# Kernel tuning notes

Measured on AMD Instinct MI355X. Metric: run time of the kernel, lower is better.

Reference implementation:

```python
import jax, jax.numpy as jnp
import numpy as np

K = 3          # kernel size
SH, SW = 2, 1  # stride
PH, PW = 1, 1  # padding


def conv2d(x, w, b, stride, pad):
    y = jax.lax.conv_general_dilated(
        x, w, window_strides=stride,
        padding=[(pad[0], pad[0]), (pad[1], pad[1])],
        dimension_numbers=('NCHW', 'OIHW', 'NCHW'))
    return y + b[None, :, None, None]


def setup_inputs() -> dict:
    key = jax.random.key(0)
    ks = jax.random.split(key, 4)
    x = jax.random.normal(ks[0], (8, 64, 128, 128), jnp.float32)
    # scale offset weights small so sampled offsets are O(1) pixels (exercises
    # the bilinear path without sampling far out of bounds)
    w_offset = jax.random.normal(ks[1], (18, 64, 3, 3), jnp.float32) * 0.02
    b_offset = jnp.zeros((18,), jnp.float32)
    w_mask = jax.random.normal(ks[2], (9, 64, 3, 3), jnp.float32) * 0.05
    b_mask = jnp.zeros((9,), jnp.float32)
    w_conv = jax.random.normal(ks[3], (64, 64, 3, 3), jnp.float32) * (1.0 / 24.0)
    return dict(x=x, w_offset=w_offset, b_offset=b_offset,
                w_mask=w_mask, b_mask=b_mask, w_conv=w_conv)


def _bilinear_gather(x, py, px):
    # x: [B,C,H,W]; py, px: [B,K2,Ho,Wo] float sampling coordinates.
    # Zero-padding outside the image (torchvision deform_conv2d semantics).
    B, C, H, W = x.shape
    y0f = jnp.floor(py)
    x0f = jnp.floor(px)
    dy = py - y0f
    dx = px - x0f
    y0 = y0f.astype(jnp.int32)
    x0 = x0f.astype(jnp.int32)

    def corner(yi, xi, wgt):
        valid = (yi >= 0) & (yi < H) & (xi >= 0) & (xi < W)
        yc = jnp.clip(yi, 0, H - 1)
        xc = jnp.clip(xi, 0, W - 1)
        # per-batch fancy gather -> [B, C, K2, Ho, Wo]
        g = jax.vmap(lambda xb, yb, xbi: xb[:, yb, xbi])(x, yc, xc)
        return g * (wgt * valid)[:, None]

    return (corner(y0,     x0,     (1 - dy) * (1 - dx))
            + corner(y0,     x0 + 1, (1 - dy) * dx)
            + corner(y0 + 1, x0,     dy * (1 - dx))
            + corner(y0 + 1, x0 + 1, dy * dx))


def reference(x, w_offset, b_offset, w_mask, b_mask, w_conv):
    B, C, H, W = x.shape
    offset = conv2d(x, w_offset, b_offset, (SH, SW), (PH, PW))   # [B, 2*K2, Ho, Wo]
    mask = jax.nn.sigmoid(conv2d(x, w_mask, b_mask, (SH, SW), (PH, PW)))  # [B, K2, Ho, Wo]
    Ho, Wo = offset.shape[2], offset.shape[3]
    K2 = K * K
    off = offset.reshape(B, K2, 2, Ho, Wo)
    off_y = off[:, :, 0]   # [B,K2,Ho,Wo]
    off_x = off[:, :, 1]
    ky = (jnp.arange(K2) // K).astype(jnp.float32)
    kx = (jnp.arange(K2) % K).astype(jnp.float32)
    hs = (jnp.arange(Ho) * SH - PH).astype(jnp.float32)
    ws = (jnp.arange(Wo) * SW - PW).astype(jnp.float32)
    py = off_y + ky[None, :, None, None] + hs[None, None, :, None]
    px = off_x + kx[None, :, None, None] + ws[None, None, None, :]
    sampled = _bilinear_gather(x, py, px) * mask[:, None]  # [B,C,K2,Ho,Wo]
    # weighted accumulate over in-channels and kernel taps
    out = jnp.einsum('ock,bckhw->bohw', w_conv.reshape(-1, C, K2), sampled)
    return out
```

## Files before the change

### kernel.cpp

```cpp
#include <hip/hip_runtime.h>
#include <hip/hip_fp16.h>
#include <math.h>

#define BB 8
#define CC 64
#define HH 128
#define WW 128
#define HO 64
#define WO 128
#define OC 64
#define HW (HH * WW)

typedef __attribute__((ext_vector_type(4))) float floatx4;
typedef __attribute__((ext_vector_type(8))) _Float16 half8;

__device__ __forceinline__ unsigned short f2h(float f) {
    __half h = __float2half(f);
    return __builtin_bit_cast(unsigned short, h);
}
__device__ __forceinline__ unsigned int packpair(float a, float b) {
    __half2 h = __floats2half2_rn(a, b);
    return __builtin_bit_cast(unsigned int, h);
}
__device__ __forceinline__ void lgkm_barrier() {
    asm volatile("s_waitcnt lgkmcnt(0)" ::: "memory");
    __builtin_amdgcn_s_barrier();
}

__global__ __launch_bounds__(256) void prep(
    const float* __restrict__ x,
    const float* __restrict__ w_off, const float* __restrict__ w_msk,
    const float* __restrict__ w_conv,
    unsigned int* __restrict__ xP,
    unsigned short* __restrict__ Wom, unsigned short* __restrict__ W2)
{
    __shared__ float T[66][65];
    int tid = threadIdx.x, bx = blockIdx.x;
    if (bx < 2048) {
        int wh = bx & 1, b = (bx >> 1) & 7, y = bx >> 4;
        int w0 = wh << 6;
        const float* xb = x + (((size_t)b * CC) * HH + y) * WW + w0;
#pragma unroll
        for (int i = 0; i < 4; ++i) {
            int idx = i * 256 + tid;
            int cch = idx >> 4, f4 = (idx & 15) << 2;
            floatx4 v = *(const floatx4*)(xb + (size_t)cch * HW + f4);
            T[f4 + 0][cch] = v.x;
            T[f4 + 1][cch] = v.y;
            T[f4 + 2][cch] = v.z;
            T[f4 + 3][cch] = v.w;
        }
        if (tid < 64) {
            float e = 0.0f;
            if (w0 + 64 < WW) e = xb[(size_t)tid * HW + 64];
            T[64][tid] = e;
        }
        __syncthreads();
        int c4 = tid & 15;
        int wr = tid >> 4;
        size_t rowbase = (((size_t)b * HH + y) * WW) + w0;
#pragma unroll
        for (int j = 0; j < 4; ++j) {
            int w = 16 * j + wr;
            floatx4 a  = *(const floatx4*)&T[w][4 * c4];
            floatx4 bb = *(const floatx4*)&T[w + 1][4 * c4];
            uint4 d;
            d.x = packpair(a.x, bb.x);
            d.y = packpair(a.y, bb.y);
            d.z = packpair(a.z, bb.z);
            d.w = packpair(a.w, bb.w);
            *(uint4*)(xP + (rowbase + w) * 64 + 4 * c4) = d;
        }
    } else if (bx < 2120) {
        int i = (bx - 2048) * 256 + tid;
        int chn = i / 576, kk = i % 576;
        int xs = kk >> 6, cc = kk & 63;
        float v = 0.0f;
        if (chn < 18)      v = w_off[(chn * CC + cc) * 9 + xs];
        else if (chn < 27) v = w_msk[((chn - 18) * CC + cc) * 9 + xs];
        Wom[i] = f2h(v);
    } else {
        int i = (bx - 2120) * 256 + tid;
        int k = i % 9, cc = (i / 9) % CC, o = i / (CC * 9);
        W2[((size_t)k * OC + o) * CC + cc] = f2h(w_conv[i]);
    }
}

__global__ __launch_bounds__(256, 4) void fused(
    const unsigned int* __restrict__ xP,
    const unsigned short* __restrict__ Wom, const unsigned short* __restrict__ W2,
    const float* __restrict__ b_off, const float* __restrict__ b_msk,
    float* __restrict__ out)
{
    __shared__ __align__(16) char lds[18304];
    typedef _Float16 XsRow[34][72];
    XsRow* Xs = (XsRow*)lds;
    unsigned short (*S)[32][64] = (unsigned short(*)[32][64])lds;
    uint2* metaC = (uint2*)(lds + 8192);
    uint2* metaR = (uint2*)(lds + 10496);
    float (*omr)[33] = (float(*)[33])(lds + 14720);

    int tid = threadIdx.x;
    int lane = tid & 63;
    int wv = __builtin_amdgcn_readfirstlane(tid >> 6);
    int bx = blockIdx.x;
    int b = bx & 7;
    int rest = bx >> 3;
    int h = rest >> 2;
    int w0 = (rest & 3) * 32;
    int h2 = 2 * h - 1;
    int m16 = lane & 15, q = lane >> 4;

    const unsigned int* xPb_u = xP + (size_t)b * HW * 64;

    for (int u = tid; u < 1632; u += 256) {
        int ky = u / 544;
        int rem = u - ky * 544;
        int col = rem >> 4, c4 = rem & 15;
        int hy = h2 + ky, wc = w0 - 1 + col;
        unsigned int lo0 = 0u, lo1 = 0u;
        if ((unsigned)hy < (unsigned)HH && (unsigned)wc < (unsigned)WW) {
            const uint4 g = *(const uint4*)(xPb_u + ((size_t)hy * WW + wc) * 64 + c4 * 4);
            lo0 = (g.x & 0xffffu) | (g.y << 16);
            lo1 = (g.z & 0xffffu) | (g.w << 16);
        }
        uint2* dst = (uint2*)((unsigned short*)lds + ((ky * 34 + col) * 72 + c4 * 4));
        *dst = make_uint2(lo0, lo1);
    }
    lgkm_barrier();

    {
        int mt = wv & 1, nt = wv >> 1;
        floatx4 a = (floatx4){0.f, 0.f, 0.f, 0.f};
        const _Float16* wa = (const _Float16*)Wom + (mt * 16 + m16) * 576 + q * 8;
#pragma unroll
        for (int t = 0; t < 18; ++t) {
            int xs = t >> 1, ky = xs / 3, kx = xs % 3;
            half8 af = *(const half8*)(wa + t * 32);
            half8 bf = *(const half8*)&Xs[ky][nt * 16 + m16 + kx][(t & 1) * 32 + q * 8];
            a = __builtin_amdgcn_mfma_f32_16x16x32_f16(af, bf, a, 0, 0, 0);
        }
#pragma unroll
        for (int r = 0; r < 4; ++r) {
            int chn = mt * 16 + q * 4 + r;
            if (chn < 27) omr[chn][nt * 16 + m16] = a[r];
        }
    }
    lgkm_barrier();

    for (int u = tid; u < 288; u += 256) {
        int kk = u >> 5, pos = u & 31;
        float offy = omr[2 * kk][pos] + b_off[2 * kk];
        float offx = omr[2 * kk + 1][pos] + b_off[2 * kk + 1];
        float mk = 1.0f / (1.0f + __expf(-(omr[18 + kk][pos] + b_msk[kk])));
        float py = offy + (float)(kk / 3) + (float)h2;
        float px = offx + (float)(kk % 3) + (float)(w0 + pos - 1);

        float y0f = floorf(py), x0f = floorf(px);
        float dy = py - y0f, dx = px - x0f;
        int y0 = (int)y0f, x0 = (int)x0f;
        int y1 = y0 + 1, x1 = x0 + 1;
        bool vy0 = (unsigned)y0 < (unsigned)HH;
        bool vy1 = (unsigned)y1 < (unsigned)HH;
        bool vx0 = (unsigned)x0 < (unsigned)WW;
        bool vx1 = (unsigned)x1 < (unsigned)WW;
        float w00 = (1.0f - dy) * (1.0f - dx) * ((vy0 && vx0) ? mk : 0.0f);
        float w01 = (1.0f - dy) * dx          * ((vy0 && vx1) ? mk : 0.0f);
        float w10 = dy * (1.0f - dx)          * ((vy1 && vx0) ? mk : 0.0f);
        float w11 = dy * dx                   * ((vy1 && vx1) ? mk : 0.0f);
        int xbase = min(max(x0, 0), WW - 2);
        bool s0 = x0 > xbase;
        bool s1 = x1 > xbase;
        float cxA = (s0 ? 0.f : w00) + (s1 ? 0.f : w01);
        float cyA = (s0 ? w00 : 0.f) + (s1 ? w01 : 0.f);
        float cxB = (s0 ? 0.f : w10) + (s1 ? 0.f : w11);
        float cyB = (s0 ? w10 : 0.f) + (s1 ? w11 : 0.f);
        int yc0 = min(max(y0, 0), HH - 1);
        int yc1 = min(max(y1, 0), HH - 1);

        __half2 hA = __floats2half2_rn(cxA, cyA);
        __half2 hB = __floats2half2_rn(cxB, cyB);
        metaC[u] = make_uint2(__builtin_bit_cast(unsigned int, hA),
                              __builtin_bit_cast(unsigned int, hB));
        metaR[u] = make_uint2((unsigned)(yc0 * WW + xbase) * 256u,
                              (unsigned)(yc1 * WW + xbase) * 256u);
    }
    lgkm_barrier();

    int p0 = wv * 8;
    const char* xPb = (const char*)xPb_u;
    unsigned int voff = 4u * (unsigned)lane;
    floatx4 acc0 = (floatx4){0.f, 0.f, 0.f, 0.f};
    floatx4 acc1 = (floatx4){0.f, 0.f, 0.f, 0.f};

    unsigned int Ga0[8], Ga1[8], Gb0[8], Gb1[8];
    half8 afr[3][2];
    const _Float16* W2w = (const _Float16*)W2 + ((size_t)wv * 16 + m16) * CC + q * 8;

    unsigned sRx[2][8], sRy[2][8];

    auto loadaf = [&](int k, int slot) {
#pragma unroll
        for (int s = 0; s < 2; ++s)
            afr[slot][s] = *(const half8*)(W2w + (size_t)k * (OC * CC) + s * 32);
    };
    auto fetchMeta = [&](int k, int s) {
#pragma unroll
        for (int i = 0; i < 8; ++i) {
            uint2 zw = metaR[k * 32 + p0 + i];
            sRx[s][i] = (unsigned)__builtin_amdgcn_readfirstlane((int)zw.x);
            sRy[s][i] = (unsigned)__builtin_amdgcn_readfirstlane((int)zw.y);
        }
    };
    auto issue = [&](int k, unsigned int (&A0)[8], unsigned int (&A1)[8]) {
        int s = k & 1;
#pragma unroll
        for (int i = 0; i < 8; ++i) {
            A0[i] = *(const unsigned int*)(xPb + sRx[s][i] + voff);
            A1[i] = *(const unsigned int*)(xPb + sRy[s][i] + voff);
        }
    };
    auto dostore = [&](int k, int buf, unsigned int (&A0)[8], unsigned int (&A1)[8]) {
#pragma unroll
        for (int i = 0; i < 8; ++i) {
            uint2 cf = metaC[k * 32 + p0 + i];
            __half2 hA = __builtin_bit_cast(__half2, cf.x);
            __half2 hB = __builtin_bit_cast(__half2, cf.y);
            __half2 g0 = __builtin_bit_cast(__half2, A0[i]);
            __half2 g1 = __builtin_bit_cast(__half2, A1[i]);
            __half2 p = __hfma2(hA, g0, __hmul2(hB, g1));
            __half sv = __hadd(__low2half(p), __high2half(p));
            int pos = p0 + i;
            S[buf][pos][((lane >> 3) ^ (pos & 7)) * 8 + (lane & 7)] =
                __builtin_bit_cast(unsigned short, sv);
        }
    };
    auto mfma_step = [&](int k, int buf, int slot) {
#pragma unroll
        for (int s = 0; s < 2; ++s) {
            half8 af = afr[slot][s];
            int cb = ((q + 4 * s) ^ (m16 & 7)) * 8;
            half8 bf0 = *(const half8*)&S[buf][m16][cb];
            half8 bf1 = *(const half8*)&S[buf][16 + m16][cb];
            acc0 = __builtin_amdgcn_mfma_f32_16x16x32_f16(af, bf0, acc0, 0, 0, 0);
            acc1 = __builtin_amdgcn_mfma_f32_16x16x32_f16(af, bf1, acc1, 0, 0, 0);
        }
    };

    loadaf(0, 0);
    loadaf(1, 1);
    fetchMeta(0, 0);
    fetchMeta(1, 1);
    issue(0, Ga0, Ga1);
    dostore(0, 0, Ga0, Ga1);
    fetchMeta(2, 0);
    issue(1, Gb0, Gb1);
#pragma unroll
    for (int k = 0; k < 9; ++k) {
        lgkm_barrier();
        if (k < 7) {
            loadaf(k + 2, (k + 2) % 3);
            if ((k & 1) == 0) issue(k + 2, Ga0, Ga1);
            else              issue(k + 2, Gb0, Gb1);
        }
        if (k < 6) fetchMeta(k + 3, (k + 3) & 1);
        mfma_step(k, k & 1, k % 3);
        if (k < 8) {
            if ((k & 1) == 0) dostore(k + 1, 1, Gb0, Gb1);
            else              dostore(k + 1, 0, Ga0, Ga1);
        }
    }

#pragma unroll
    for (int nt = 0; nt < 2; ++nt) {
        floatx4 av = nt ? acc1 : acc0;
#pragma unroll
        for (int r = 0; r < 4; ++r) {
            int o = wv * 16 + q * 4 + r;
            out[(((size_t)b * OC + o) * HO + h) * WO + w0 + nt * 16 + m16] = av[r];
        }
    }
}

extern "C" void kernel_launch(void* const* d_in, const int* in_sizes, int n_in,
                              void* d_out, int out_size, void* d_ws, size_t ws_size,
                              hipStream_t stream)
{
    const float* x      = (const float*)d_in[0];
    const float* w_off  = (const float*)d_in[1];
    const float* b_off  = (const float*)d_in[2];
    const float* w_msk  = (const float*)d_in[3];
    const float* b_msk  = (const float*)d_in[4];
    const float* w_conv = (const float*)d_in[5];
    float* out = (float*)d_out;

    unsigned int* xP = (unsigned int*)d_ws;
    unsigned short* Wom = (unsigned short*)(xP + (size_t)BB * HW * 64);
    unsigned short* W2 = Wom + 32 * 576;

    prep<<<dim3(2264), dim3(256), 0, stream>>>(x, w_off, w_msk, w_conv,
                                               xP, Wom, W2);
    fused<<<dim3(2048), dim3(256), 0, stream>>>(xP, Wom, W2,
                                                b_off, b_msk, out);
}
```

Baseline: 142.0 us.

## Merge prep and fused kernels into one persistent kernel with grid barrier

Combines the layout-conversion prep kernel and the main deformable-conv kernel into a single launch of 1024 blocks, separated by a software grid-wide barrier on an atomic counter. Each block now converts two half-rows of input and then handles two output tiles in a loop. Meta readfirstlane fetches are folded into the gather issue, dropping the separate scalar prefetch pipeline. This removes a kernel launch and the gap between the kernels. In exchange it adds a memset, a spin barrier that needs all 1024 blocks resident at once, and less overlap between the prefetch stages.

```diff
diff --git a/kernel.cpp b/kernel.cpp
--- a/kernel.cpp
+++ b/kernel.cpp
@@ -10,6 +10,7 @@
 #define WO 128
 #define OC 64
 #define HW (HH * WW)
+#define NBLOCKS 1024u
 
 typedef __attribute__((ext_vector_type(4))) float floatx4;
 typedef __attribute__((ext_vector_type(8))) _Float16 half8;
@@ -26,73 +27,93 @@
     asm volatile("s_waitcnt lgkmcnt(0)" ::: "memory");
     __builtin_amdgcn_s_barrier();
 }
-
-__global__ __launch_bounds__(256) void prep(
+__device__ __forceinline__ void grid_sync(unsigned* cnt) {
+    __syncthreads();
+    if (threadIdx.x == 0) {
+        __threadfence();
+        atomicAdd(cnt, 1u);
+        unsigned guard = 0;
+        while (atomicAdd(cnt, 0u) < NBLOCKS && guard < (1u << 24)) {
+            __builtin_amdgcn_s_sleep(8);
+            ++guard;
+        }
+    }
+    __syncthreads();
+    __threadfence();
+}
+
+__global__ __launch_bounds__(256, 4) void merged(
     const float* __restrict__ x,
     const float* __restrict__ w_off, const float* __restrict__ w_msk,
     const float* __restrict__ w_conv,
+    const float* __restrict__ b_off, const float* __restrict__ b_msk,
     unsigned int* __restrict__ xP,
-    unsigned short* __restrict__ Wom, unsigned short* __restrict__ W2)
+    unsigned short* __restrict__ Wom, unsigned short* __restrict__ W2,
+    unsigned* __restrict__ syncnt,
+    float* __restrict__ out)
 {
-    __shared__ float T[66][65];
-    int tid = threadIdx.x, bx = blockIdx.x;
-    if (bx < 2048) {
-        int wh = bx & 1, b = (bx >> 1) & 7, y = bx >> 4;
-        int w0 = wh << 6;
-        const float* xb = x + (((size_t)b * CC) * HH + y) * WW + w0;
-#pragma unroll
-        for (int i = 0; i < 4; ++i) {
-            int idx = i * 256 + tid;
-            int cch = idx >> 4, f4 = (idx & 15) << 2;
-            floatx4 v = *(const floatx4*)(xb + (size_t)cch * HW + f4);
-            T[f4 + 0][cch] = v.x;
-            T[f4 + 1][cch] = v.y;
-            T[f4 + 2][cch] = v.z;
-            T[f4 + 3][cch] = v.w;
-        }
-        if (tid < 64) {
-            float e = 0.0f;
-            if (w0 + 64 < WW) e = xb[(size_t)tid * HW + 64];
-            T[64][tid] = e;
-        }
-        __syncthreads();
-        int c4 = tid & 15;
-        int wr = tid >> 4;
-        size_t rowbase = (((size_t)b * HH + y) * WW) + w0;
-#pragma unroll
-        for (int j = 0; j < 4; ++j) {
-            int w = 16 * j + wr;
-            floatx4 a  = *(const floatx4*)&T[w][4 * c4];
-            floatx4 bb = *(const floatx4*)&T[w + 1][4 * c4];
-            uint4 d;
-            d.x = packpair(a.x, bb.x);
-            d.y = packpair(a.y, bb.y);
-            d.z = packpair(a.z, bb.z);
-            d.w = packpair(a.w, bb.w);
-            *(uint4*)(xP + (rowbase + w) * 64 + 4 * c4) = d;
-        }
-    } else if (bx < 2120) {
-        int i = (bx - 2048) * 256 + tid;
-        int chn = i / 576, kk = i % 576;
+    __shared__ __align__(16) char lds[18432];
+    int tid = threadIdx.x;
+    int i = blockIdx.x;
+
+    if (i < 72) {
+        int u = i * 256 + tid;
+        int chn = u / 576, kk = u % 576;
         int xs = kk >> 6, cc = kk & 63;
         float v = 0.0f;
         if (chn < 18)      v = w_off[(chn * CC + cc) * 9 + xs];
         else if (chn < 27) v = w_msk[((chn - 18) * CC + cc) * 9 + xs];
-        Wom[i] = f2h(v);
-    } else {
-        int i = (bx - 2120) * 256 + tid;
-        int k = i % 9, cc = (i / 9) % CC, o = i / (CC * 9);
-        W2[((size_t)k * OC + o) * CC + cc] = f2h(w_conv[i]);
+        Wom[u] = f2h(v);
+    } else if (i < 216) {
+        int u = (i - 72) * 256 + tid;
+        int k = u % 9, cc = (u / 9) % CC, o = u / (CC * 9);
+        W2[((size_t)k * OC + o) * CC + cc] = f2h(w_conv[u]);
     }
-}
-
-__global__ __launch_bounds__(256, 4) void fused(
-    const unsigned int* __restrict__ xP,
-    const unsigned short* __restrict__ Wom, const unsigned short* __restrict__ W2,
-    const float* __restrict__ b_off, const float* __restrict__ b_msk,
-    float* __restrict__ out)
-{
-    __shared__ __align__(16) char lds[18304];
+
+    {
+        float (*T)[65] = (float(*)[65])lds;
+        int bs = i & 7, y = i >> 3;
+#pragma unroll 1
+        for (int j = 0; j < 2; ++j) {
+            __syncthreads();
+            int w0 = j << 6;
+            const float* xb = x + (((size_t)bs * CC) * HH + y) * WW + w0;
+#pragma unroll
+            for (int it = 0; it < 4; ++it) {
+                int idx = it * 256 + tid;
+                int cch = idx >> 4, f4 = (idx & 15) << 2;
+                floatx4 v = *(const floatx4*)(xb + (size_t)cch * HW + f4);
+                T[f4 + 0][cch] = v.x;
+                T[f4 + 1][cch] = v.y;
+                T[f4 + 2][cch] = v.z;
+                T[f4 + 3][cch] = v.w;
+            }
+            if (tid < 64) {
+                float e = 0.0f;
+                if (w0 + 64 < WW) e = xb[(size_t)tid * HW + 64];
+                T[64][tid] = e;
+            }
+            __syncthreads();
+            int c4 = tid & 15;
+            int wr = tid >> 4;
+            size_t rowbase = (((size_t)bs * HH + y) * WW) + w0;
+#pragma unroll
+            for (int jj = 0; jj < 4; ++jj) {
+                int w = 16 * jj + wr;
+                floatx4 a  = *(const floatx4*)&T[w][4 * c4];
+                floatx4 bb = *(const floatx4*)&T[w + 1][4 * c4];
+                uint4 d;
+                d.x = packpair(a.x, bb.x);
+                d.y = packpair(a.y, bb.y);
+                d.z = packpair(a.z, bb.z);
+                d.w = packpair(a.w, bb.w);
+                *(uint4*)(xP + (rowbase + w) * 64 + 4 * c4) = d;
+            }
+        }
+    }
+
+    grid_sync(syncnt);
+
     typedef _Float16 XsRow[34][72];
     XsRow* Xs = (XsRow*)lds;
     unsigned short (*S)[32][64] = (unsigned short(*)[32][64])lds;
@@ -100,184 +121,176 @@
     uint2* metaR = (uint2*)(lds + 10496);
     float (*omr)[33] = (float(*)[33])(lds + 14720);
 
-    int tid = threadIdx.x;
     int lane = tid & 63;
     int wv = __builtin_amdgcn_readfirstlane(tid >> 6);
-    int bx = blockIdx.x;
-    int b = bx & 7;
-    int rest = bx >> 3;
-    int h = rest >> 2;
-    int w0 = (rest & 3) * 32;
+    int b = i & 7;
+    int rest = i >> 3;
+    int h = rest >> 1;
+    int wt2 = rest & 1;
     int h2 = 2 * h - 1;
     int m16 = lane & 15, q = lane >> 4;
 
     const unsigned int* xPb_u = xP + (size_t)b * HW * 64;
-
-    for (int u = tid; u < 1632; u += 256) {
-        int ky = u / 544;
-        int rem = u - ky * 544;
-        int col = rem >> 4, c4 = rem & 15;
-        int hy = h2 + ky, wc = w0 - 1 + col;
-        unsigned int lo0 = 0u, lo1 = 0u;
-        if ((unsigned)hy < (unsigned)HH && (unsigned)wc < (unsigned)WW) {
-            const uint4 g = *(const uint4*)(xPb_u + ((size_t)hy * WW + wc) * 64 + c4 * 4);
-            lo0 = (g.x & 0xffffu) | (g.y << 16);
-            lo1 = (g.z & 0xffffu) | (g.w << 16);
-        }
-        uint2* dst = (uint2*)((unsigned short*)lds + ((ky * 34 + col) * 72 + c4 * 4));
-        *dst = make_uint2(lo0, lo1);
-    }
-    lgkm_barrier();
-
-    {
-        int mt = wv & 1, nt = wv >> 1;
-        floatx4 a = (floatx4){0.f, 0.f, 0.f, 0.f};
-        const _Float16* wa = (const _Float16*)Wom + (mt * 16 + m16) * 576 + q * 8;
-#pragma unroll
-        for (int t = 0; t < 18; ++t) {
-            int xs = t >> 1, ky = xs / 3, kx = xs % 3;
-            half8 af = *(const half8*)(wa + t * 32);
-            half8 bf = *(const half8*)&Xs[ky][nt * 16 + m16 + kx][(t & 1) * 32 + q * 8];
-            a = __builtin_amdgcn_mfma_f32_16x16x32_f16(af, bf, a, 0, 0, 0);
-        }
-#pragma unroll
-        for (int r = 0; r < 4; ++r) {
-            int chn = mt * 16 + q * 4 + r;
-            if (chn < 27) omr[chn][nt * 16 + m16] = a[r];
-        }
-    }
-    lgkm_barrier();
-
-    for (int u = tid; u < 288; u += 256) {
-        int kk = u >> 5, pos = u & 31;
-        float offy = omr[2 * kk][pos] + b_off[2 * kk];
-        float offx = omr[2 * kk + 1][pos] + b_off[2 * kk + 1];
-        float mk = 1.0f / (1.0f + __expf(-(omr[18 + kk][pos] + b_msk[kk])));
-        float py = offy + (float)(kk / 3) + (float)h2;
-        float px = offx + (float)(kk % 3) + (float)(w0 + pos - 1);
-
-        float y0f = floorf(py), x0f = floorf(px);
-        float dy = py - y0f, dx = px - x0f;
-        int y0 = (int)y0f, x0 = (int)x0f;
-        int y1 = y0 + 1, x1 = x0 + 1;
-        bool vy0 = (unsigned)y0 < (unsigned)HH;
-        bool vy1 = (unsigned)y1 < (unsigned)HH;
-        bool vx0 = (unsigned)x0 < (unsigned)WW;
-        bool vx1 = (unsigned)x1 < (unsigned)WW;
-        float w00 = (1.0f - dy) * (1.0f - dx) * ((vy0 && vx0) ? mk : 0.0f);
-        float w01 = (1.0f - dy) * dx          * ((vy0 && vx1) ? mk : 0.0f);
-        float w10 = dy * (1.0f - dx)          * ((vy1 && vx0) ? mk : 0.0f);
-        float w11 = dy * dx                   * ((vy1 && vx1) ? mk : 0.0f);
-        int xbase = min(max(x0, 0), WW - 2);
-        bool s0 = x0 > xbase;
-        bool s1 = x1 > xbase;
-        float cxA = (s0 ? 0.f : w00) + (s1 ? 0.f : w01);
-        float cyA = (s0 ? w00 : 0.f) + (s1 ? w01 : 0.f);
-        float cxB = (s0 ? 0.f : w10) + (s1 ? 0.f : w11);
-        float cyB = (s0 ? w10 : 0.f) + (s1 ? w11 : 0.f);
-        int yc0 = min(max(y0, 0), HH - 1);
-        int yc1 = min(max(y1, 0), HH - 1);
-
-        __half2 hA = __floats2half2_rn(cxA, cyA);
-        __half2 hB = __floats2half2_rn(cxB, cyB);
-        metaC[u] = make_uint2(__builtin_bit_cast(unsigned int, hA),
-                              __builtin_bit_cast(unsigned int, hB));
-        metaR[u] = make_uint2((unsigned)(yc0 * WW + xbase) * 256u,
-                              (unsigned)(yc1 * WW + xbase) * 256u);
-    }
-    lgkm_barrier();
-
-    int p0 = wv * 8;
     const char* xPb = (const char*)xPb_u;
     unsigned int voff = 4u * (unsigned)lane;
-    floatx4 acc0 = (floatx4){0.f, 0.f, 0.f, 0.f};
-    floatx4 acc1 = (floatx4){0.f, 0.f, 0.f, 0.f};
-
-    unsigned int Ga0[8], Ga1[8], Gb0[8], Gb1[8];
-    half8 afr[3][2];
-    const _Float16* W2w = (const _Float16*)W2 + ((size_t)wv * 16 + m16) * CC + q * 8;
-
-    unsigned sRx[2][8], sRy[2][8];
-
-    auto loadaf = [&](int k, int slot) {
-#pragma unroll
-        for (int s = 0; s < 2; ++s)
-            afr[slot][s] = *(const half8*)(W2w + (size_t)k * (OC * CC) + s * 32);
-    };
-    auto fetchMeta = [&](int k, int s) {
-#pragma unroll
-        for (int i = 0; i < 8; ++i) {
-            uint2 zw = metaR[k * 32 + p0 + i];
-            sRx[s][i] = (unsigned)__builtin_amdgcn_readfirstlane((int)zw.x);
-            sRy[s][i] = (unsigned)__builtin_amdgcn_readfirstlane((int)zw.y);
-        }
-    };
-    auto issue = [&](int k, unsigned int (&A0)[8], unsigned int (&A1)[8]) {
-        int s = k & 1;
-#pragma unroll
-        for (int i = 0; i < 8; ++i) {
-            A0[i] = *(const unsigned int*)(xPb + sRx[s][i] + voff);
-            A1[i] = *(const unsigned int*)(xPb + sRy[s][i] + voff);
-        }
-    };
-    auto dostore = [&](int k, int buf, unsigned int (&A0)[8], unsigned int (&A1)[8]) {
-#pragma unroll
-        for (int i = 0; i < 8; ++i) {
-            uint2 cf = metaC[k * 32 + p0 + i];
-            __half2 hA = __builtin_bit_cast(__half2, cf.x);
-            __half2 hB = __builtin_bit_cast(__half2, cf.y);
-            __half2 g0 = __builtin_bit_cast(__half2, A0[i]);
-            __half2 g1 = __builtin_bit_cast(__half2, A1[i]);
-            __half2 p = __hfma2(hA, g0, __hmul2(hB, g1));
-            __half sv = __hadd(__low2half(p), __high2half(p));
-            int pos = p0 + i;
-            S[buf][pos][((lane >> 3) ^ (pos & 7)) * 8 + (lane & 7)] =
-                __builtin_bit_cast(unsigned short, sv);
-        }
-    };
-    auto mfma_step = [&](int k, int buf, int slot) {
-#pragma unroll
-        for (int s = 0; s < 2; ++s) {
-            half8 af = afr[slot][s];
-            int cb = ((q + 4 * s) ^ (m16 & 7)) * 8;
-            half8 bf0 = *(const half8*)&S[buf][m16][cb];
-            half8 bf1 = *(const half8*)&S[buf][16 + m16][cb];
-            acc0 = __builtin_amdgcn_mfma_f32_16x16x32_f16(af, bf0, acc0, 0, 0, 0);
-            acc1 = __builtin_amdgcn_mfma_f32_16x16x32_f16(af, bf1, acc1, 0, 0, 0);
-        }
-    };
-
-    loadaf(0, 0);
-    loadaf(1, 1);
-    fetchMeta(0, 0);
-    fetchMeta(1, 1);
-    issue(0, Ga0, Ga1);
-    dostore(0, 0, Ga0, Ga1);
-    fetchMeta(2, 0);
-    issue(1, Gb0, Gb1);
-#pragma unroll
-    for (int k = 0; k < 9; ++k) {
+
+#pragma unroll 1
+    for (int t2 = 0; t2 < 2; ++t2) {
+        int w0 = (wt2 * 2 + t2) * 32;
         lgkm_barrier();
-        if (k < 7) {
-            loadaf(k + 2, (k + 2) % 3);
-            if ((k & 1) == 0) issue(k + 2, Ga0, Ga1);
-            else              issue(k + 2, Gb0, Gb1);
-        }
-        if (k < 6) fetchMeta(k + 3, (k + 3) & 1);
-        mfma_step(k, k & 1, k % 3);
-        if (k < 8) {
-            if ((k & 1) == 0) dostore(k + 1, 1, Gb0, Gb1);
-            else              dostore(k + 1, 0, Ga0, Ga1);
-        }
-    }
-
-#pragma unroll
-    for (int nt = 0; nt < 2; ++nt) {
-        floatx4 av = nt ? acc1 : acc0;
-#pragma unroll
-        for (int r = 0; r < 4; ++r) {
-            int o = wv * 16 + q * 4 + r;
-            out[(((size_t)b * OC + o) * HO + h) * WO + w0 + nt * 16 + m16] = av[r];
+
+        for (int u = tid; u < 1632; u += 256) {
+            int ky = u / 544;
+            int rem = u - ky * 544;
+            int col = rem >> 4, c4 = rem & 15;
+            int hy = h2 + ky, wc = w0 - 1 + col;
+            unsigned int lo0 = 0u, lo1 = 0u;
+            if ((unsigned)hy < (unsigned)HH && (unsigned)wc < (unsigned)WW) {
+                const uint4 g = *(const uint4*)(xPb_u + ((size_t)hy * WW + wc) * 64 + c4 * 4);
+                lo0 = (g.x & 0xffffu) | (g.y << 16);
+                lo1 = (g.z & 0xffffu) | (g.w << 16);
+            }
+            uint2* dst = (uint2*)((unsigned short*)lds + ((ky * 34 + col) * 72 + c4 * 4));
+            *dst = make_uint2(lo0, lo1);
+        }
+        lgkm_barrier();
+
+        {
+            int mt = wv & 1, nt = wv >> 1;
+            floatx4 a = (floatx4){0.f, 0.f, 0.f, 0.f};
+            const _Float16* wa = (const _Float16*)Wom + (mt * 16 + m16) * 576 + q * 8;
+#pragma unroll
+            for (int t = 0; t < 18; ++t) {
+                int xs = t >> 1, ky = xs / 3, kx = xs % 3;
+                half8 af = *(const half8*)(wa + t * 32);
+                half8 bf = *(const half8*)&Xs[ky][nt * 16 + m16 + kx][(t & 1) * 32 + q * 8];
+                a = __builtin_amdgcn_mfma_f32_16x16x32_f16(af, bf, a, 0, 0, 0);
+            }
+#pragma unroll
+            for (int r = 0; r < 4; ++r) {
+                int chn = mt * 16 + q * 4 + r;
+                if (chn < 27) omr[chn][nt * 16 + m16] = a[r];
+            }
+        }
+        lgkm_barrier();
+
+        for (int u = tid; u < 288; u += 256) {
+            int kk = u >> 5, pos = u & 31;
+            float offy = omr[2 * kk][pos] + b_off[2 * kk];
+            float offx = omr[2 * kk + 1][pos] + b_off[2 * kk + 1];
+            float mk = 1.0f / (1.0f + __expf(-(omr[18 + kk][pos] + b_msk[kk])));
+            float py = offy + (float)(kk / 3) + (float)h2;
+            float px = offx + (float)(kk % 3) + (float)(w0 + pos - 1);
+
+            float y0f = floorf(py), x0f = floorf(px);
+            float dy = py - y0f, dx = px - x0f;
+            int y0 = (int)y0f, x0 = (int)x0f;
+            int y1 = y0 + 1, x1 = x0 + 1;
+            bool vy0 = (unsigned)y0 < (unsigned)HH;
+            bool vy1 = (unsigned)y1 < (unsigned)HH;
+            bool vx0 = (unsigned)x0 < (unsigned)WW;
+            bool vx1 = (unsigned)x1 < (unsigned)WW;
+            float w00 = (1.0f - dy) * (1.0f - dx) * ((vy0 && vx0) ? mk : 0.0f);
+            float w01 = (1.0f - dy) * dx          * ((vy0 && vx1) ? mk : 0.0f);
+            float w10 = dy * (1.0f - dx)          * ((vy1 && vx0) ? mk : 0.0f);
+            float w11 = dy * dx                   * ((vy1 && vx1) ? mk : 0.0f);
+            int xbase = min(max(x0, 0), WW - 2);
+            bool s0 = x0 > xbase;
+            bool s1 = x1 > xbase;
+            float cxA = (s0 ? 0.f : w00) + (s1 ? 0.f : w01);
+            float cyA = (s0 ? w00 : 0.f) + (s1 ? w01 : 0.f);
+            float cxB = (s0 ? 0.f : w10) + (s1 ? 0.f : w11);
+            float cyB = (s0 ? w10 : 0.f) + (s1 ? w11 : 0.f);
+            int yc0 = min(max(y0, 0), HH - 1);
+            int yc1 = min(max(y1, 0), HH - 1);
+
+            __half2 hA = __floats2half2_rn(cxA, cyA);
+            __half2 hB = __floats2half2_rn(cxB, cyB);
+            metaC[u] = make_uint2(__builtin_bit_cast(unsigned int, hA),
+                                  __builtin_bit_cast(unsigned int, hB));
+            metaR[u] = make_uint2((unsigned)(yc0 * WW + xbase) * 256u,
+                                  (unsigned)(yc1 * WW + xbase) * 256u);
+        }
+        lgkm_barrier();
+
+        int p0 = wv * 8;
+        floatx4 acc0 = (floatx4){0.f, 0.f, 0.f, 0.f};
+        floatx4 acc1 = (floatx4){0.f, 0.f, 0.f, 0.f};
+
+        unsigned int Ga0[8], Ga1[8], Gb0[8], Gb1[8];
+        half8 afr[3][2];
+        const _Float16* W2w = (const _Float16*)W2 + ((size_t)wv * 16 + m16) * CC + q * 8;
+
+        auto loadaf = [&](int k, int slot) {
+#pragma unroll
+            for (int s = 0; s < 2; ++s)
+                afr[slot][s] = *(const half8*)(W2w + (size_t)k * (OC * CC) + s * 32);
+        };
+        auto issue = [&](int k, unsigned int (&A0)[8], unsigned int (&A1)[8]) {
+#pragma unroll
+            for (int ii = 0; ii < 8; ++ii) {
+                uint2 zw = metaR[k * 32 + p0 + ii];
+                const char* r0 = xPb + (unsigned)__builtin_amdgcn_readfirstlane((int)zw.x);
+                const char* r1 = xPb + (unsigned)__builtin_amdgcn_readfirstlane((int)zw.y);
+                A0[ii] = *(const unsigned int*)(r0 + voff);
+                A1[ii] = *(const unsigned int*)(r1 + voff);
+            }
+        };
+        auto dostore = [&](int k, int buf, unsigned int (&A0)[8], unsigned int (&A1)[8]) {
+#pragma unroll
+            for (int ii = 0; ii < 8; ++ii) {
+                uint2 cf = metaC[k * 32 + p0 + ii];
+                __half2 hA = __builtin_bit_cast(__half2, cf.x);
+                __half2 hB = __builtin_bit_cast(__half2, cf.y);
+                __half2 g0 = __builtin_bit_cast(__half2, A0[ii]);
+                __half2 g1 = __builtin_bit_cast(__half2, A1[ii]);
+                __half2 p = __hfma2(hA, g0, __hmul2(hB, g1));
+                __half sv = __hadd(__low2half(p), __high2half(p));
+                int pos = p0 + ii;
+                S[buf][pos][((lane >> 3) ^ (pos & 7)) * 8 + (lane & 7)] =
+                    __builtin_bit_cast(unsigned short, sv);
+            }
+        };
+        auto mfma_step = [&](int k, int buf, int slot) {
+#pragma unroll
+            for (int s = 0; s < 2; ++s) {
+                half8 af = afr[slot][s];
+                int cb = ((q + 4 * s) ^ (m16 & 7)) * 8;
+                half8 bf0 = *(const half8*)&S[buf][m16][cb];
+                half8 bf1 = *(const half8*)&S[buf][16 + m16][cb];
+                acc0 = __builtin_amdgcn_mfma_f32_16x16x32_f16(af, bf0, acc0, 0, 0, 0);
+                acc1 = __builtin_amdgcn_mfma_f32_16x16x32_f16(af, bf1, acc1, 0, 0, 0);
+            }
+        };
+
+        loadaf(0, 0);
+        loadaf(1, 1);
+        issue(0, Ga0, Ga1);
+        dostore(0, 0, Ga0, Ga1);
+        issue(1, Gb0, Gb1);
+#pragma unroll
+        for (int k = 0; k < 9; ++k) {
+            lgkm_barrier();
+            if (k < 7) {
+                loadaf(k + 2, (k + 2) % 3);
+                if ((k & 1) == 0) issue(k + 2, Ga0, Ga1);
+                else              issue(k + 2, Gb0, Gb1);
+            }
+            mfma_step(k, k & 1, k % 3);
+            if (k < 8) {
+                if ((k & 1) == 0) dostore(k + 1, 1, Gb0, Gb1);
+                else              dostore(k + 1, 0, Ga0, Ga1);
+            }
+        }
+
+#pragma unroll
+        for (int nt = 0; nt < 2; ++nt) {
+            floatx4 av = nt ? acc1 : acc0;
+#pragma unroll
+            for (int r = 0; r < 4; ++r) {
+                int o = wv * 16 + q * 4 + r;
+                out[(((size_t)b * OC + o) * HO + h) * WO + w0 + nt * 16 + m16] = av[r];
+            }
         }
     }
 }
@@ -297,9 +310,9 @@
     unsigned int* xP = (unsigned int*)d_ws;
     unsigned short* Wom = (unsigned short*)(xP + (size_t)BB * HW * 64);
     unsigned short* W2 = Wom + 32 * 576;
-
-    prep<<<dim3(2264), dim3(256), 0, stream>>>(x, w_off, w_msk, w_conv,
-                                               xP, Wom, W2);
-    fused<<<dim3(2048), dim3(256), 0, stream>>>(xP, Wom, W2,
-                                                b_off, b_msk, out);
-}
+    unsigned* syncnt = (unsigned*)((char*)(W2 + 36864));
+
+    hipMemsetAsync(syncnt, 0, 64, stream);
+    merged<<<dim3(NBLOCKS), dim3(256), 0, stream>>>(
+        x, w_off, w_msk, w_conv, b_off, b_msk, xP, Wom, W2, syncnt, out);
+}
```

New measurement: 308.7 us. 2.17x slower.
